# Performance work log

Measured on AMD Instinct MI355X. Metric: run time of the kernel, lower is better.

Reference implementation:

```python
import jax, jax.numpy as jnp
import numpy as np

T, B, E, H = 2048, 2, 1024, 16
D = E // H
MAX_REL = 16  # RelativePosition default max_relative_position


def setup_inputs() -> dict:
    key = jax.random.key(0)
    ks = jax.random.split(key, 11)
    s = 1.0 / np.sqrt(E)
    inp = {
        'query': jax.random.normal(ks[0], (T, B, E), dtype=jnp.float32),
        'Wq': jax.random.normal(ks[1], (E, E), dtype=jnp.float32) * s,
        'bq': jnp.zeros((E,), dtype=jnp.float32),
        'Wk': jax.random.normal(ks[2], (E, E), dtype=jnp.float32) * s,
        'bk': jnp.zeros((E,), dtype=jnp.float32),
        'Wv': jax.random.normal(ks[3], (E, E), dtype=jnp.float32) * s,
        'bv': jnp.zeros((E,), dtype=jnp.float32),
        'Wo': jax.random.normal(ks[4], (E, E), dtype=jnp.float32) * s,
        'bo': jnp.zeros((E,), dtype=jnp.float32),
        'rk_table': jax.random.normal(ks[5], (2 * MAX_REL + 1, D), dtype=jnp.float32) * 0.05,
        'rv_table': jax.random.normal(ks[6], (2 * MAX_REL + 1, D), dtype=jnp.float32) * 0.05,
    }
    return inp


def _rel_idx(lq, lk):
    # distance_mat = k - q, clipped to [-MAX_REL, MAX_REL], shifted to [0, 2*MAX_REL]
    d = jnp.arange(lk)[None, :] - jnp.arange(lq)[:, None]
    return jnp.clip(d, -MAX_REL, MAX_REL) + MAX_REL  # [lq, lk] int


def reference(query, Wq, bq, Wk, bk, Wv, bv, Wo, bo, rk_table, rv_table):
    t, b, e = query.shape
    scale = D ** -0.5
    # projections (torch Linear: x @ W.T + b)
    q = (query @ Wq.T + bq) * scale
    k = query @ Wk.T + bk
    v = query @ Wv.T + bv
    # [T,B,E] -> [B*H, T, D]
    q = q.reshape(t, b * H, D).transpose(1, 0, 2)
    k = k.reshape(t, b * H, D).transpose(1, 0, 2)
    v = v.reshape(t, b * H, D).transpose(1, 0, 2)
    # content scores + Shaw relative-position key scores
    scores = jnp.einsum('ntd,nsd->nts', q, k)            # [N, T, S]
    rk = rk_table[_rel_idx(t, t)]                        # [T, S, D]
    scores = scores + jnp.einsum('ntd,tsd->nts', q, rk)  # relpos_k term
    probs = jax.nn.softmax(scores, axis=-1)
    # weighted values + Shaw relative-position value term
    rv = rv_table[_rel_idx(t, t)]                        # [T, S, D]
    attn = jnp.einsum('nts,nsd->ntd', probs, v) + jnp.einsum('nts,tsd->ntd', probs, rv)
    # [B*H, T, D] -> [T, B, E]
    attn = attn.transpose(1, 0, 2).reshape(t, b, e)
    return attn @ Wo.T + bo
```

## Files before the change

### kernel.cpp

```cpp
#include <hip/hip_runtime.h>
#include <hip/hip_bf16.h>
#include <math.h>

#define T_   2048
#define B_   2
#define E_   1024
#define H_   16
#define D_   64
#define NH_  32
#define M_   4096

typedef __attribute__((ext_vector_type(8))) short s8b;
typedef __attribute__((ext_vector_type(4))) float f4;

#define MFMA_B16(a,b,c) __builtin_amdgcn_mfma_f32_16x16x32_bf16(a,b,c,0,0,0)
#define LOG2E 1.44269504088896f

__device__ __forceinline__ unsigned short f2bu(float f) {
    union { __hip_bfloat16 h; unsigned short u; } cv;
    cv.h = __float2bfloat16(f);
    return cv.u;
}
__device__ __forceinline__ unsigned short f2bu_fast(float f) {
    return (unsigned short)((__float_as_uint(f) + 0x8000u) >> 16);
}
__device__ __forceinline__ float bu2f(unsigned short u) {
    union { __hip_bfloat16 h; unsigned short u; } cv; cv.u = u;
    return __bfloat162float(cv.h);
}
__device__ __forceinline__ unsigned int pk2(float a, float b) {
    return (unsigned int)f2bu(a) | ((unsigned int)f2bu(b) << 16);
}
__device__ __forceinline__ unsigned int pk2_fast(float a, float b) {
    return ((__float_as_uint(a) + 0x8000u) >> 16) |
           ((__float_as_uint(b) + 0x8000u) & 0xFFFF0000u);
}
__device__ __forceinline__ float fexp2(float x) {
    return __builtin_amdgcn_exp2f(x);
}
__device__ __forceinline__ float ld1d(const void* p, size_t idx, bool f32) {
    return f32 ? ((const float*)p)[idx] : bu2f(((const unsigned short*)p)[idx]);
}
__device__ __forceinline__ float qsumq(float v) {
    v += __shfl_xor(v, 16); v += __shfl_xor(v, 32);
    return v;
}
__device__ __forceinline__ void glds16(const unsigned short* g, unsigned short* l) {
    __builtin_amdgcn_global_load_lds(
        (const __attribute__((address_space(1))) unsigned int*)g,
        (__attribute__((address_space(3))) unsigned int*)l, 16, 0, 0);
}
__device__ __forceinline__ bool detect_f32(const unsigned short* q16) {
    int e = (q16[threadIdx.x & 63] >> 7) & 0xFF;
    bool sane = (e == 0) || (e >= 97 && e <= 157);
    unsigned long long m = __ballot(sane);
    return __popcll(m) < 56;
}

__global__ __launch_bounds__(256) void cvt_bf16(
    const void* __restrict__ x,
    const void* __restrict__ Wq, const void* __restrict__ Wk,
    const void* __restrict__ Wv, const void* __restrict__ Wo,
    const void* __restrict__ bq, const void* __restrict__ bk,
    const void* __restrict__ bv, const void* __restrict__ bo,
    unsigned short* __restrict__ xw, unsigned short* __restrict__ Ww,
    unsigned short* __restrict__ bw, int* __restrict__ flag)
{
    const bool f32m = detect_f32((const unsigned short*)x);
    if (blockIdx.x == 0 && blockIdx.y == 0 && threadIdx.x == 0)
        *flag = f32m ? 1 : 0;
    const int y = blockIdx.y;
    const void* src; unsigned short* dst; int n;
    if (y == 0)      { src = x; dst = xw; n = M_ * E_; }
    else if (y <= 4) {
        src = (y == 1) ? Wq : (y == 2) ? Wk : (y == 3) ? Wv : Wo;
        dst = Ww + (size_t)(y - 1) * E_ * E_; n = E_ * E_;
    } else {
        src = (y == 5) ? bq : (y == 6) ? bk : (y == 7) ? bv : bo;
        dst = bw + (size_t)(y - 5) * E_; n = E_;
    }
    int i = (blockIdx.x * 256 + threadIdx.x) * 8;
    if (i >= n) return;
    if (f32m) {
        const float* s = (const float*)src + i;
        float4 f0 = *(const float4*)s, f1 = *(const float4*)(s + 4);
        union { unsigned int d[4]; s8b v; } u;
        u.d[0] = pk2(f0.x, f0.y); u.d[1] = pk2(f0.z, f0.w);
        u.d[2] = pk2(f1.x, f1.y); u.d[3] = pk2(f1.z, f1.w);
        *(s8b*)(dst + i) = u.v;
    } else {
        *(s8b*)(dst + i) = *(const s8b*)((const unsigned short*)src + i);
    }
}

__global__ __launch_bounds__(256, 3) void qkv_gemm(
    const unsigned short* __restrict__ xw, const unsigned short* __restrict__ Ww,
    const unsigned short* __restrict__ bw,
    unsigned short* __restrict__ qo, unsigned short* __restrict__ ko,
    unsigned short* __restrict__ vo)
{
    const int bid = blockIdx.x;
    const int r_ = bid & 7, s_ = bid >> 3;
    const int g = r_ + 8 * (s_ >> 3);
    const int e0 = (s_ & 7) * 128;
    const int m0 = (g & 31) * 128;
    const int p  = g >> 5;
    const unsigned short* W    = Ww + (size_t)p * E_ * E_;
    const unsigned short* bias = bw + (size_t)p * E_;
    const float scale = (p == 0) ? 0.125f * LOG2E : 1.0f;

    const int tid = threadIdx.x, w = tid >> 6, lane = tid & 63;
    const int quad = lane >> 4, lc = lane & 15;
    const int wx = w & 1, wy = w >> 1;

    __shared__ unsigned short smem[4][128 * 32];

    f4 acc[4][4];
    #pragma unroll
    for (int i = 0; i < 4; i++)
        #pragma unroll
        for (int j = 0; j < 4; j++) acc[i][j] = (f4){0.f, 0.f, 0.f, 0.f};

    const int gr = lane >> 2;
    const int gc = (lane & 3) ^ ((lane >> 2) & 3);
    const size_t aoff = (size_t)(m0 + w*32 + gr) * E_ + gc*8;
    const size_t boff = (size_t)(e0 + w*32 + gr) * E_ + gc*8;

    #pragma unroll
    for (int j = 0; j < 2; j++) {
        glds16(xw + aoff + (size_t)j*16*E_, &smem[0][(w*128 + j*64) * 8]);
        glds16(W  + boff + (size_t)j*16*E_, &smem[2][(w*128 + j*64) * 8]);
    }
    __syncthreads();

    const int fcA = quad ^ (lc & 3);
    for (int k0 = 0; k0 < E_; k0 += 32) {
        const int cur = (k0 >> 5) & 1;
        if (k0 + 32 < E_) {
            #pragma unroll
            for (int j = 0; j < 2; j++) {
                glds16(xw + aoff + (size_t)j*16*E_ + k0 + 32, &smem[cur^1][(w*128 + j*64) * 8]);
                glds16(W  + boff + (size_t)j*16*E_ + k0 + 32, &smem[2 + (cur^1)][(w*128 + j*64) * 8]);
            }
        }
        s8b af[4], bfr[4];
        #pragma unroll
        for (int i = 0; i < 4; i++)
            af[i]  = *(const s8b*)&smem[cur][((wy*64 + i*16 + lc)*4 + fcA) * 8];
        #pragma unroll
        for (int i = 0; i < 4; i++)
            bfr[i] = *(const s8b*)&smem[2 + cur][((wx*64 + i*16 + lc)*4 + fcA) * 8];
        #pragma unroll
        for (int ms = 0; ms < 4; ms++)
            #pragma unroll
            for (int ns = 0; ns < 4; ns++)
                acc[ms][ns] = MFMA_B16(af[ms], bfr[ns], acc[ms][ns]);
        __syncthreads();
    }

    float bias_v[4];
    #pragma unroll
    for (int ns = 0; ns < 4; ns++) bias_v[ns] = bu2f(bias[e0 + wx*64 + ns*16 + lc]);

    if (p < 2) {
        #pragma unroll
        for (int ms = 0; ms < 4; ms++)
            #pragma unroll
            for (int ns = 0; ns < 4; ns++)
                #pragma unroll
                for (int r2 = 0; r2 < 4; r2++) {
                    float val = (acc[ms][ns][r2] + bias_v[ns]) * scale;
                    float nb = __shfl_xor(val, 1);
                    if (!(lane & 1)) {
                        int m = m0 + wy*64 + ms*16 + quad*4 + r2;
                        int t = m >> 1, bb = m & 1;
                        int e = e0 + wx*64 + ns*16 + lc;
                        int h = e >> 6, d = e & 63;
                        unsigned short* dst = (p == 0) ? qo : ko;
                        *(unsigned int*)&dst[(((size_t)(bb*H_ + h) * T_ + t) << 6) + d] = pk2(val, nb);
                    }
                }
    } else {
        unsigned int* cst = (unsigned int*)&smem[0][0];
        #pragma unroll
        for (int ms = 0; ms < 4; ms++) {
            const int tq = wy*16 + ms*4 + quad;
            #pragma unroll
            for (int ns = 0; ns < 4; ns++) {
                const int e_l = wx*64 + ns*16 + lc;
                const int x = (e_l & 7) << 2;
                float v0 = acc[ms][ns][0] + bias_v[ns];
                float v1 = acc[ms][ns][1] + bias_v[ns];
                float v2 = acc[ms][ns][2] + bias_v[ns];
                float v3 = acc[ms][ns][3] + bias_v[ns];
                cst[e_l*64 + ( tq       ^ x)] = pk2(v0, v2);
                cst[e_l*64 + ((32 + tq) ^ x)] = pk2(v1, v3);
            }
        }
        __syncthreads();
        #pragma unroll
        for (int i = 0; i < 8; i++) {
            const int li  = i*256 + tid;
            const int e_l = li >> 4;
            const int bb  = (li >> 3) & 1;
            const int ch  = li & 7;
            const int x   = (e_l & 7) << 2;
            uint4 vd = *(const uint4*)&cst[e_l*64 + ((bb*32 + ch*4) ^ x)];
            const int e = e0 + e_l, h = e >> 6, d = e & 63;
            const size_t du = ((size_t)(bb*H_ + h) * 64 + d) * (T_/2)
                              + (m0 >> 2) + ch*4;
            *(uint4*)((unsigned int*)vo + du) = vd;
        }
    }
}

__global__ __launch_bounds__(512, 4) void attn_mfma(
    const unsigned short* __restrict__ q, const unsigned short* __restrict__ k,
    const unsigned short* __restrict__ v,
    const void* __restrict__ rk_t, const void* __restrict__ rv_t,
    unsigned short* __restrict__ aout, const int* __restrict__ flag)
{
    const bool f32m = (*flag != 0);
    const int bid = blockIdx.x;
    const int n = bid & 31, qt = bid >> 5;
    const int t0 = qt * 128;
    const int tid = threadIdx.x, w = tid >> 6, lane = tid & 63;
    const int quad = lane >> 4, lc = lane & 15;

    __shared__ unsigned short k_s[2][64 * 64];
    __shared__ unsigned short v_s[2][64 * 64];
    __shared__ unsigned short p_s[8][16 * 72];
    __shared__ unsigned short qrk_s[128 * 36];
    __shared__ unsigned short diag16[128 * 33];
    __shared__ float st_L[128], st_R[128];

    const unsigned short* qn = q + ((size_t)n * T_ + t0) * D_;
    const unsigned short* kn = k + (size_t)n * T_ * D_;
    const unsigned short* vn = v + (size_t)n * D_ * T_;

    s8b qa[2];
    #pragma unroll
    for (int kf = 0; kf < 2; kf++)
        qa[kf] = *(const s8b*)(qn + (size_t)(w*16 + lc) * D_ + kf*32 + quad*8);

    for (int i = tid; i < 128 * 33; i += 512) diag16[i] = 0;

    unsigned int* rks = (unsigned int*)&p_s[0][0];
    for (int i = tid; i < 48 * 36; i += 512) {
        int r = i / 36, c2 = i % 36;
        unsigned int val = 0;
        if (r < 33 && c2 < 32)
            val = pk2(ld1d(rk_t, r*64 + 2*c2, f32m), ld1d(rk_t, r*64 + 2*c2 + 1, f32m));
        rks[i] = val;
    }
    __syncthreads();

    for (int nt = 0; nt < 3; nt++) {
        s8b b0 = *(const s8b*)((const unsigned short*)rks + (nt*16 + lc)*72 + quad*8);
        s8b b1 = *(const s8b*)((const unsigned short*)rks + (nt*16 + lc)*72 + 32 + quad*8);
        f4 a = (f4){0.f, 0.f, 0.f, 0.f};
        a = MFMA_B16(qa[0], b0, a);
        a = MFMA_B16(qa[1], b1, a);
        #pragma unroll
        for (int r = 0; r < 4; r++) {
            float nb = __shfl_xor(a[r], 1);
            int col = nt*16 + lc;
            if (!(lane & 1) && col < 34)
                ((unsigned int*)qrk_s)[(w*16 + quad*4 + r)*18 + (col >> 1)] = pk2(a[r], nb);
        }
    }
    __syncthreads();

    const int t_l = w*16 + lc;
    const float qLn = bu2f(qrk_s[t_l*36 + 0]);
    const float qRn = bu2f(qrk_s[t_l*36 + 32]);
    float L_p = 0.f, R_p = 0.f;
    f4 O[4], lsN, lsL, lsR;
    lsN = (f4){0.f, 0.f, 0.f, 0.f};
    lsL = (f4){0.f, 0.f, 0.f, 0.f};
    lsR = (f4){0.f, 0.f, 0.f, 0.f};
    #pragma unroll
    for (int dt = 0; dt < 4; dt++) O[dt] = (f4){0.f, 0.f, 0.f, 0.f};
    const short ob = (short)0x3F80;
    const s8b ones = { ob, ob, ob, ob, ob, ob, ob, ob };

    const int grr = lane >> 3;
    const int gcc = (lane & 7) ^ grr;
    const size_t koff = (size_t)(w*8 + grr) * D_ + gcc*8;
    const size_t voff = (size_t)(w*8 + grr) * T_ + gcc*8;

    const int kts = ((bid >> 8) & 1) * 16;

    s8b kr0 = *(const s8b*)(kn + koff + (size_t)(kts * 64) * D_);
    s8b vr0 = *(const s8b*)(vn + voff + kts * 64);
    *(s8b*)&k_s[0][(w*64 + lane) * 8] = kr0;
    *(s8b*)&v_s[0][(w*64 + lane) * 8] = vr0;
    __syncthreads();

    const int lc7 = lc & 7;
    for (int it = 0; it < 32; it++) {
        const int kt = (it + kts) & 31;
        const int s0 = kt * 64;
        const int cur = it & 1;
        if (it + 1 < 32) {
            const int s0n = ((it + 1 + kts) & 31) * 64;
            kr0 = *(const s8b*)(kn + koff + (size_t)s0n * D_);
            vr0 = *(const s8b*)(vn + voff + s0n);
        }

        const bool farL  = (s0 + 63 < t0 - 16);
        const bool farR  = (s0 > t0 + 143);
        const bool nearT = !farL && !farR;

        s8b ak[4][2];
        #pragma unroll
        for (int st = 0; st < 4; st++) {
            int row = st*16 + lc;
            ak[st][0] = *(const s8b*)&k_s[cur][(row*8 + (quad       ^ lc7)) * 8];
            ak[st][1] = *(const s8b*)&k_s[cur][(row*8 + ((4 + quad) ^ lc7)) * 8];
        }

        #pragma unroll
        for (int st = 0; st < 4; st++) {
            f4 a;
            if (nearT) a = (f4){0.f, 0.f, 0.f, 0.f};
            else {
                float qb = farL ? qLn : qRn;
                a = (f4){qb, qb, qb, qb};
            }
            a = MFMA_B16(ak[st][0], qa[0], a);
            a = MFMA_B16(ak[st][1], qa[1], a);
            unsigned int lo, hi;
            if (nearT) {
                const int sb = s0 + st*16 + quad*4 - (t0 + t_l);
                unsigned short eb[4];
                #pragma unroll
                for (int r = 0; r < 4; r++) {
                    int rel = sb + r;
                    int rc = rel < -16 ? -16 : (rel > 16 ? 16 : rel);
                    float e = fexp2(a[r] + bu2f(qrk_s[t_l*36 + rc + 16]));
                    eb[r] = f2bu_fast(e);
                    if (rel <= -16)      L_p += e;
                    else if (rel >= 16)  R_p += e;
                    else                 diag16[t_l*33 + rel + 15] = eb[r];
                }
                lo = (unsigned int)eb[0] | ((unsigned int)eb[1] << 16);
                hi = (unsigned int)eb[2] | ((unsigned int)eb[3] << 16);
            } else {
                lo = pk2_fast(fexp2(a[0]), fexp2(a[1]));
                hi = pk2_fast(fexp2(a[2]), fexp2(a[3]));
            }
            *(uint2*)&p_s[w][lc*72 + st*16 + quad*4] = make_uint2(lo, hi);
        }

        s8b pb[2];
        pb[0] = *(const s8b*)&p_s[w][lc*72 + quad*8];
        pb[1] = *(const s8b*)&p_s[w][lc*72 + 32 + quad*8];
        if (nearT) {
            lsN = MFMA_B16(ones, pb[0], lsN);
            lsN = MFMA_B16(ones, pb[1], lsN);
        } else if (farL) {
            lsL = MFMA_B16(ones, pb[0], lsL);
            lsL = MFMA_B16(ones, pb[1], lsL);
        } else {
            lsR = MFMA_B16(ones, pb[0], lsR);
            lsR = MFMA_B16(ones, pb[1], lsR);
        }
        #pragma unroll
        for (int dt = 0; dt < 4; dt++) {
            int row = dt*16 + lc;
            s8b a0 = *(const s8b*)&v_s[cur][(row*8 + (quad       ^ lc7)) * 8];
            s8b a1 = *(const s8b*)&v_s[cur][(row*8 + ((4 + quad) ^ lc7)) * 8];
            O[dt] = MFMA_B16(a0, pb[0], O[dt]);
            O[dt] = MFMA_B16(a1, pb[1], O[dt]);
        }

        if (it + 1 < 32) {
            *(s8b*)&k_s[cur ^ 1][(w*64 + lane) * 8] = kr0;
            *(s8b*)&v_s[cur ^ 1][(w*64 + lane) * 8] = vr0;
        }
        __syncthreads();
    }

    float l = lsN[0] + lsL[0] + lsR[0];
    float L = lsL[0] + qsumq(L_p);
    float R = lsR[0] + qsumq(R_p);
    const float linv = 1.f / l;
    if (quad == 0) { st_L[t_l] = L; st_R[t_l] = R; }
    {
        unsigned int* rvs = (unsigned int*)&k_s[0][0];
        for (int i = tid; i < 64 * 32; i += 512) {
            int d = i >> 5, dwL = i & 31;
            int r0 = dwL * 2, r1 = r0 + 1;
            float x0 = (r0 < 33) ? ld1d(rv_t, (size_t)r0 * 64 + d, f32m) : 0.f;
            float x1 = (r1 < 33) ? ld1d(rv_t, (size_t)r1 * 64 + d, f32m) : 0.f;
            int phys = d * 32 + ((dwL >> 2) ^ (d & 7)) * 4 + (dwL & 3);
            rvs[phys] = pk2(x0, x1);
        }
    }
    __syncthreads();
    for (int j = 0; j < 16; j++) {
        int c = lane;
        int row = w*16 + j;
        unsigned short pv;
        if (c == 0)        pv = f2bu(st_L[row]);
        else if (c == 32)  pv = f2bu(st_R[row]);
        else if (c < 32)   pv = diag16[row*33 + c - 1];
        else               pv = 0;
        p_s[w][j*72 + c] = pv;
    }
    s8b pe[2];
    pe[0] = *(const s8b*)&p_s[w][lc*72 + quad*8];
    pe[1] = *(const s8b*)&p_s[w][lc*72 + 32 + quad*8];
    #pragma unroll
    for (int dt = 0; dt < 4; dt++) {
        int row = dt*16 + lc;
        s8b a0 = *(const s8b*)&k_s[0][(row*8 + (quad       ^ lc7)) * 8];
        s8b a1 = *(const s8b*)&k_s[0][(row*8 + ((4 + quad) ^ lc7)) * 8];
        O[dt] = MFMA_B16(a0, pe[0], O[dt]);
        O[dt] = MFMA_B16(a1, pe[1], O[dt]);
    }
    const int bb = n >> 4, h = n & 15;
    {
        int t_g = t0 + t_l;
        #pragma unroll
        for (int dt = 0; dt < 4; dt++) {
            float v0 = O[dt][0] * linv;
            float v1 = O[dt][1] * linv;
            float v2 = O[dt][2] * linv;
            float v3 = O[dt][3] * linv;
            int e = h*64 + dt*16 + quad*4;
            *(uint2*)&aout[((size_t)t_g * B_ + bb) * E_ + e] =
                make_uint2(pk2(v0, v1), pk2(v2, v3));
        }
    }
}

__global__ __launch_bounds__(256, 3) void out_gemm(
    const unsigned short* __restrict__ A,
    const unsigned short* __restrict__ Wob, const unsigned short* __restrict__ bob,
    void* __restrict__ out, const int* __restrict__ flag)
{
    const bool f32m = (*flag != 0);
    const int bid = blockIdx.x;
    const int r_ = bid & 7, s_ = bid >> 3;
    const int g = r_ + 8 * (s_ >> 3);
    const int m0 = g * 128;
    const int e0 = (s_ & 7) * 128;

    const int tid = threadIdx.x, w = tid >> 6, lane = tid & 63;
    const int quad = lane >> 4, lc = lane & 15;
    const int wx = w & 1, wy = w >> 1;

    __shared__ unsigned short a_s[2][128 * 32];
    __shared__ unsigned short b_s[2][128 * 32];

    f4 acc[4][4];
    #pragma unroll
    for (int i = 0; i < 4; i++)
        #pragma unroll
        for (int j = 0; j < 4; j++) acc[i][j] = (f4){0.f, 0.f, 0.f, 0.f};

    const int gr = lane >> 2;
    const int gc = (lane & 3) ^ ((lane >> 2) & 3);
    const size_t aoff = (size_t)(m0 + w*32 + gr) * E_ + gc*8;
    const size_t boff = (size_t)(e0 + w*32 + gr) * E_ + gc*8;

    #pragma unroll
    for (int j = 0; j < 2; j++) {
        glds16(A   + aoff + (size_t)j*16*E_, &a_s[0][(w*128 + j*64) * 8]);
        glds16(Wob + boff + (size_t)j*16*E_, &b_s[0][(w*128 + j*64) * 8]);
    }
    __syncthreads();

    const int fcA = quad ^ (lc & 3);
    for (int k0 = 0; k0 < E_; k0 += 32) {
        const int cur = (k0 >> 5) & 1;
        if (k0 + 32 < E_) {
            #pragma unroll
            for (int j = 0; j < 2; j++) {
                glds16(A   + aoff + (size_t)j*16*E_ + k0 + 32, &a_s[cur^1][(w*128 + j*64) * 8]);
                glds16(Wob + boff + (size_t)j*16*E_ + k0 + 32, &b_s[cur^1][(w*128 + j*64) * 8]);
            }
        }
        s8b af[4], bfr[4];
        #pragma unroll
        for (int i = 0; i < 4; i++)
            af[i]  = *(const s8b*)&a_s[cur][((wy*64 + i*16 + lc)*4 + fcA) * 8];
        #pragma unroll
        for (int i = 0; i < 4; i++)
            bfr[i] = *(const s8b*)&b_s[cur][((wx*64 + i*16 + lc)*4 + fcA) * 8];
        #pragma unroll
        for (int ms = 0; ms < 4; ms++)
            #pragma unroll
            for (int ns = 0; ns < 4; ns++)
                acc[ms][ns] = MFMA_B16(af[ms], bfr[ns], acc[ms][ns]);
        __syncthreads();
    }

    float bias_v[4];
    #pragma unroll
    for (int ns = 0; ns < 4; ns++) bias_v[ns] = bu2f(bob[e0 + wx*64 + ns*16 + lc]);

    #pragma unroll
    for (int ms = 0; ms < 4; ms++)
        #pragma unroll
        for (int ns = 0; ns < 4; ns++)
            #pragma unroll
            for (int r2 = 0; r2 < 4; r2++) {
                float val = acc[ms][ns][r2] + bias_v[ns];
                size_t m = m0 + wy*64 + ms*16 + quad*4 + r2;
                int e = e0 + wx*64 + ns*16 + lc;
                if (f32m) {
                    ((float*)out)[m * E_ + e] = val;
                } else {
                    float nb = __shfl_xor(val, 1);
                    if (!(lane & 1))
                        *(unsigned int*)&((unsigned short*)out)[m * E_ + e] = pk2(val, nb);
                }
            }
}

extern "C" void kernel_launch(void* const* d_in, const int* in_sizes, int n_in,
                              void* d_out, int out_size, void* d_ws, size_t ws_size,
                              hipStream_t stream) {
    const void* x  = d_in[0];
    const void* Wq = d_in[1];  const void* bq = d_in[2];
    const void* Wk = d_in[3];  const void* bk = d_in[4];
    const void* Wv = d_in[5];  const void* bv = d_in[6];
    const void* Wo = d_in[7];  const void* bo = d_in[8];
    const void* rk = d_in[9];  const void* rv = d_in[10];

    int* flag = (int*)d_ws;
    const size_t HTD = (size_t)NH_ * T_ * D_;
    unsigned short* qw = (unsigned short*)((char*)d_ws + 256);
    unsigned short* kw = qw + HTD;
    unsigned short* vw = kw + HTD;
    unsigned short* aw = vw + HTD;
    unsigned short* xw = aw + (size_t)M_ * E_;
    unsigned short* Ww = xw + (size_t)M_ * E_;
    unsigned short* bw = Ww + (size_t)4 * E_ * E_;

    cvt_bf16<<<dim3((M_*E_/8 + 255)/256, 9), 256, 0, stream>>>(
        x, Wq, Wk, Wv, Wo, bq, bk, bv, bo, xw, Ww, bw, flag);
    qkv_gemm<<<dim3(768), 256, 0, stream>>>(xw, Ww, bw, qw, kw, vw);
    attn_mfma<<<dim3(NH_ * (T_/128)), 512, 0, stream>>>(qw, kw, vw, rk, rv, aw, flag);
    out_gemm<<<dim3(256), 256, 0, stream>>>(aw, Ww + (size_t)3*E_*E_, bw + 3*E_,
                                            d_out, flag);
}
```

Measured before the change: 216.5 us.

## Compact cvt grid and stage GEMM epilogues through LDS for coalesced stores

New measurement: 207.8 us. -4.0%, faster.

```diff
diff --git a/kernel.cpp b/kernel.cpp
--- a/kernel.cpp
+++ b/kernel.cpp
@@ -67,9 +67,13 @@
     unsigned short* __restrict__ bw, int* __restrict__ flag)
 {
     const bool f32m = detect_f32((const unsigned short*)x);
-    if (blockIdx.x == 0 && blockIdx.y == 0 && threadIdx.x == 0)
+    const int bid = blockIdx.x;
+    if (bid == 0 && threadIdx.x == 0)
         *flag = f32m ? 1 : 0;
-    const int y = blockIdx.y;
+    int y, lb;
+    if (bid < 2048)       { y = 0;                      lb = bid; }
+    else if (bid < 4096)  { y = 1 + ((bid - 2048) >> 9); lb = (bid - 2048) & 511; }
+    else                  { y = 5 + (bid - 4096);        lb = 0; }
     const void* src; unsigned short* dst; int n;
     if (y == 0)      { src = x; dst = xw; n = M_ * E_; }
     else if (y <= 4) {
@@ -79,7 +83,7 @@
         src = (y == 5) ? bq : (y == 6) ? bk : (y == 7) ? bv : bo;
         dst = bw + (size_t)(y - 5) * E_; n = E_;
     }
-    int i = (blockIdx.x * 256 + threadIdx.x) * 8;
+    int i = (lb * 256 + threadIdx.x) * 8;
     if (i >= n) return;
     if (f32m) {
         const float* s = (const float*)src + i;
@@ -162,6 +166,7 @@
     #pragma unroll
     for (int ns = 0; ns < 4; ns++) bias_v[ns] = bu2f(bias[e0 + wx*64 + ns*16 + lc]);
 
+    unsigned int* cst = (unsigned int*)&smem[0][0];
     if (p < 2) {
         #pragma unroll
         for (int ms = 0; ms < 4; ms++)
@@ -172,16 +177,27 @@
                     float val = (acc[ms][ns][r2] + bias_v[ns]) * scale;
                     float nb = __shfl_xor(val, 1);
                     if (!(lane & 1)) {
-                        int m = m0 + wy*64 + ms*16 + quad*4 + r2;
-                        int t = m >> 1, bb = m & 1;
-                        int e = e0 + wx*64 + ns*16 + lc;
-                        int h = e >> 6, d = e & 63;
-                        unsigned short* dst = (p == 0) ? qo : ko;
-                        *(unsigned int*)&dst[(((size_t)(bb*H_ + h) * T_ + t) << 6) + d] = pk2(val, nb);
+                        int mi = wy*64 + ms*16 + quad*4 + r2;
+                        int ei = wx*64 + ns*16 + lc;
+                        int row = ((mi & 1) * 2 + (ei >> 6)) * 64 + (mi >> 1);
+                        int col = (ei & 63) >> 1;
+                        cst[row*32 + (col ^ ((row & 7) << 2))] = pk2(val, nb);
                     }
                 }
+        __syncthreads();
+        unsigned int* dst32 = (unsigned int*)((p == 0) ? qo : ko);
+        #pragma unroll
+        for (int i = 0; i < 8; i++) {
+            const int li  = i*256 + tid;
+            const int row = li >> 3;
+            const int ch  = li & 7;
+            uint4 vd = *(const uint4*)&cst[row*32 + ((ch*4) ^ ((row & 7) << 2))];
+            const int bb = row >> 7, hh = (row >> 6) & 1, tq = row & 63;
+            const size_t du = (((size_t)(bb*H_ + (e0 >> 6) + hh) * T_
+                                + (m0 >> 1) + tq) << 5) + ch*4;
+            *(uint4*)&dst32[du] = vd;
+        }
     } else {
-        unsigned int* cst = (unsigned int*)&smem[0][0];
         #pragma unroll
         for (int ms = 0; ms < 4; ms++) {
             const int tq = wy*16 + ms*4 + quad;
@@ -452,8 +468,7 @@
     const int quad = lane >> 4, lc = lane & 15;
     const int wx = w & 1, wy = w >> 1;
 
-    __shared__ unsigned short a_s[2][128 * 32];
-    __shared__ unsigned short b_s[2][128 * 32];
+    __shared__ unsigned short smem[4][128 * 32];
 
     f4 acc[4][4];
     #pragma unroll
@@ -468,8 +483,8 @@
 
     #pragma unroll
     for (int j = 0; j < 2; j++) {
-        glds16(A   + aoff + (size_t)j*16*E_, &a_s[0][(w*128 + j*64) * 8]);
-        glds16(Wob + boff + (size_t)j*16*E_, &b_s[0][(w*128 + j*64) * 8]);
+        glds16(A   + aoff + (size_t)j*16*E_, &smem[0][(w*128 + j*64) * 8]);
+        glds16(Wob + boff + (size_t)j*16*E_, &smem[2][(w*128 + j*64) * 8]);
     }
     __syncthreads();
 
@@ -479,17 +494,17 @@
         if (k0 + 32 < E_) {
             #pragma unroll
             for (int j = 0; j < 2; j++) {
-                glds16(A   + aoff + (size_t)j*16*E_ + k0 + 32, &a_s[cur^1][(w*128 + j*64) * 8]);
-                glds16(Wob + boff + (size_t)j*16*E_ + k0 + 32, &b_s[cur^1][(w*128 + j*64) * 8]);
+                glds16(A   + aoff + (size_t)j*16*E_ + k0 + 32, &smem[cur^1][(w*128 + j*64) * 8]);
+                glds16(Wob + boff + (size_t)j*16*E_ + k0 + 32, &smem[2 + (cur^1)][(w*128 + j*64) * 8]);
             }
         }
         s8b af[4], bfr[4];
         #pragma unroll
         for (int i = 0; i < 4; i++)
-            af[i]  = *(const s8b*)&a_s[cur][((wy*64 + i*16 + lc)*4 + fcA) * 8];
+            af[i]  = *(const s8b*)&smem[cur][((wy*64 + i*16 + lc)*4 + fcA) * 8];
         #pragma unroll
         for (int i = 0; i < 4; i++)
-            bfr[i] = *(const s8b*)&b_s[cur][((wx*64 + i*16 + lc)*4 + fcA) * 8];
+            bfr[i] = *(const s8b*)&smem[2 + cur][((wx*64 + i*16 + lc)*4 + fcA) * 8];
         #pragma unroll
         for (int ms = 0; ms < 4; ms++)
             #pragma unroll
@@ -502,23 +517,47 @@
     #pragma unroll
     for (int ns = 0; ns < 4; ns++) bias_v[ns] = bu2f(bob[e0 + wx*64 + ns*16 + lc]);
 
-    #pragma unroll
-    for (int ms = 0; ms < 4; ms++)
-        #pragma unroll
-        for (int ns = 0; ns < 4; ns++)
-            #pragma unroll
-            for (int r2 = 0; r2 < 4; r2++) {
-                float val = acc[ms][ns][r2] + bias_v[ns];
-                size_t m = m0 + wy*64 + ms*16 + quad*4 + r2;
-                int e = e0 + wx*64 + ns*16 + lc;
-                if (f32m) {
+    if (f32m) {
+        #pragma unroll
+        for (int ms = 0; ms < 4; ms++)
+            #pragma unroll
+            for (int ns = 0; ns < 4; ns++)
+                #pragma unroll
+                for (int r2 = 0; r2 < 4; r2++) {
+                    float val = acc[ms][ns][r2] + bias_v[ns];
+                    size_t m = m0 + wy*64 + ms*16 + quad*4 + r2;
+                    int e = e0 + wx*64 + ns*16 + lc;
                     ((float*)out)[m * E_ + e] = val;
-                } else {
+                }
+    } else {
+        unsigned int* cst = (unsigned int*)&smem[0][0];
+        #pragma unroll
+        for (int ms = 0; ms < 4; ms++)
+            #pragma unroll
+            for (int ns = 0; ns < 4; ns++)
+                #pragma unroll
+                for (int r2 = 0; r2 < 4; r2++) {
+                    float val = acc[ms][ns][r2] + bias_v[ns];
                     float nb = __shfl_xor(val, 1);
-                    if (!(lane & 1))
-                        *(unsigned int*)&((unsigned short*)out)[m * E_ + e] = pk2(val, nb);
+                    if (!(lane & 1)) {
+                        int mi = wy*64 + ms*16 + quad*4 + r2;
+                        int ei = wx*64 + ns*16 + lc;
+                        int col = ei >> 1;
+                        cst[mi*64 + (col ^ ((mi & 7) << 2))] = pk2(val, nb);
+                    }
                 }
-            }
+        __syncthreads();
+        unsigned int* dst32 = (unsigned int*)out;
+        #pragma unroll
+        for (int i = 0; i < 8; i++) {
+            const int li  = i*256 + tid;
+            const int row = li >> 4;
+            const int ch  = li & 15;
+            uint4 vd = *(const uint4*)&cst[row*64 + ((ch*4) ^ ((row & 7) << 2))];
+            const size_t du = ((size_t)(m0 + row) * E_ + e0) / 2 + ch*4;
+            *(uint4*)&dst32[du] = vd;
+        }
+    }
 }
 
 extern "C" void kernel_launch(void* const* d_in, const int* in_sizes, int n_in,
@@ -541,7 +580,7 @@
     unsigned short* Ww = xw + (size_t)M_ * E_;
     unsigned short* bw = Ww + (size_t)4 * E_ * E_;
 
-    cvt_bf16<<<dim3((M_*E_/8 + 255)/256, 9), 256, 0, stream>>>(
+    cvt_bf16<<<dim3(4100), 256, 0, stream>>>(
         x, Wq, Wk, Wv, Wo, bq, bk, bv, bo, xw, Ww, bw, flag);
     qkv_gemm<<<dim3(768), 256, 0, stream>>>(xw, Ww, bw, qw, kw, vw);
     attn_mfma<<<dim3(NH_ * (T_/128)), 512, 0, stream>>>(qw, kw, vw, rk, rv, aw, flag);
```
